# Optimization experiments

Hardware: AMD Instinct MI355X
Metric: run time of the kernel (lower is better)

The kernel has to match this reference:

```python
import jax, jax.numpy as jnp
import numpy as np

U, I, D, E = 100000, 50000, 128, 3200000


def setup_inputs() -> dict:
    key = jax.random.key(0)
    k0, k1, k2, k3, k4 = jax.random.split(key, 5)
    stdv = 1.0 / np.sqrt(D)
    return {
        "user_embedding": jax.random.uniform(k0, (U, D), jnp.float32, -stdv, stdv),
        "item_embedding": jax.random.uniform(k1, (I, D), jnp.float32, -stdv, stdv),
        "edge_vals": jax.random.uniform(k2, (E,), jnp.float32),  # normalized adj values
        "edge_u": jax.random.randint(k3, (E,), 0, U, jnp.int32),
        "edge_i": jax.random.randint(k4, (E,), 0, I, jnp.int32),
        "n_layers": 3,
    }


def reference(user_embedding, item_embedding, edge_vals, edge_u, edge_i, n_layers):
    # LightGCN forward: alternate SpMM on bipartite graph G [U,I] (COO edges),
    # then average embeddings across layers 0..n_layers.
    num_users = user_embedding.shape[0]
    num_items = item_embedding.shape[0]
    u_list = [user_embedding]
    i_list = [item_embedding]
    w = edge_vals[:, None]  # [E,1]
    for layer in range(n_layers):
        # u_{l+1} = G @ i_l : gather item rows along edges, scale, scatter-add to users
        new_u = jax.ops.segment_sum(w * i_list[layer][edge_i], edge_u,
                                    num_segments=num_users)
        # i_{l+1} = G^T @ u_l
        new_i = jax.ops.segment_sum(w * u_list[layer][edge_u], edge_i,
                                    num_segments=num_items)
        u_list.append(new_u)
        i_list.append(new_i)
    denom = jnp.float32(n_layers + 1)
    embed_user = sum(u_list) / denom
    embed_item = sum(i_list) / denom
    return (embed_user, embed_item)
```

## Files before the change

### kernel.cpp

```cpp
#include <hip/hip_runtime.h>


#define D 128
#define CHUNK 8192
#define CTILE 64
#define SRCMASK 0x3FFFF
#define TPB 256
#define RS_CAP 6144
#define NSPLIT 16

typedef unsigned int u32x2 __attribute__((ext_vector_type(2)));
typedef float f32x4 __attribute__((ext_vector_type(4)));

__device__ inline uint2 ntload_u2(const uint2* p) {
    u32x2 v = __builtin_nontemporal_load((const u32x2*)p);
    uint2 r; r.x = v.x; r.y = v.y; return r;
}
__device__ inline void ntstore_f4(float* p, float4 v) {
    f32x4 t; t.x = v.x; t.y = v.y; t.z = v.z; t.w = v.w;
    __builtin_nontemporal_store(t, (f32x4*)p);
}
__device__ inline int ntload_i(const int* p) { return __builtin_nontemporal_load(p); }
__device__ inline float ntload_f(const float* p) { return __builtin_nontemporal_load(p); }
__device__ inline float4 ntload_f4(const float* p) {
    f32x4 v = __builtin_nontemporal_load((const f32x4*)p);
    return make_float4(v.x, v.y, v.z, v.w);
}

__device__ inline unsigned pack4(float a, float b, float c, float d, float qs) {
    int q0 = __float2int_rn(a * qs), q1 = __float2int_rn(b * qs);
    int q2 = __float2int_rn(c * qs), q3 = __float2int_rn(d * qs);
    return ((unsigned)(q0 & 255)) | ((unsigned)(q1 & 255) << 8) |
           ((unsigned)(q2 & 255) << 16) | ((unsigned)(q3 & 255) << 24);
}

__device__ inline void acc_q8(float4& sa, float4& sb, uint2 raw, float m) {
    unsigned x = raw.x, y = raw.y;
    sa.x += m * (float)((int)(x << 24) >> 24);
    sa.y += m * (float)((int)(x << 16) >> 24);
    sa.z += m * (float)((int)(x <<  8) >> 24);
    sa.w += m * (float)((int)(x      ) >> 24);
    sb.x += m * (float)((int)(y << 24) >> 24);
    sb.y += m * (float)((int)(y << 16) >> 24);
    sb.z += m * (float)((int)(y <<  8) >> 24);
    sb.w += m * (float)((int)(y      ) >> 24);
}

__global__ __launch_bounds__(TPB) void k_quant8(
    const float* __restrict__ ue, const float* __restrict__ ie,
    uint2* __restrict__ h0q, float* __restrict__ sc0, int U, int UA, int NP) {
    int row = blockIdx.x * (TPB / 16) + (threadIdx.x >> 4);
    if (row >= NP) return;
    int lane = threadIdx.x & 15;
    float4 a = make_float4(0.f, 0.f, 0.f, 0.f);
    float4 b = make_float4(0.f, 0.f, 0.f, 0.f);
    const float* p = nullptr;
    if (row < U)        p = ue + (size_t)row * D + lane * 8;
    else if (row >= UA) p = ie + (size_t)(row - UA) * D + lane * 8;
    if (p) { a = ntload_f4(p); b = ntload_f4(p + 4); }
    float m = fmaxf(fmaxf(fmaxf(fabsf(a.x), fabsf(a.y)), fmaxf(fabsf(a.z), fabsf(a.w))),
                    fmaxf(fmaxf(fabsf(b.x), fabsf(b.y)), fmaxf(fabsf(b.z), fabsf(b.w))));
    for (int d_ = 1; d_ < 16; d_ <<= 1) m = fmaxf(m, __shfl_xor(m, d_));
    float qs = (m > 0.f) ? 127.f / m : 0.f;
    uint2 q;
    q.x = pack4(a.x, a.y, a.z, a.w, qs);
    q.y = pack4(b.x, b.y, b.z, b.w, qs);
    h0q[(size_t)row * 16 + lane] = q;
    if (lane == 0) sc0[row] = m * (1.f / 127.f);
}

__global__ __launch_bounds__(256) void k_count(const int* __restrict__ eu,
                                               const int* __restrict__ ei,
                                               int* __restrict__ C, int* __restrict__ C2,
                                               int E, int NB, int NS, int UA) {
    extern __shared__ int hist[];
    for (int k = threadIdx.x; k < NB; k += blockDim.x) hist[k] = 0;
    __syncthreads();
    int base = blockIdx.x * CHUNK;
    int n = min(CHUNK, E - base);
    for (int t = threadIdx.x; t < n; t += blockDim.x) {
        int u = ntload_i(eu + base + t);
        int i = ntload_i(ei + base + t);
        atomicAdd(&hist[u >> 6], 1);
        atomicAdd(&hist[(UA + i) >> 6], 1);
    }
    __syncthreads();
    int* Crow = C + (size_t)blockIdx.x * NB;
    for (int k = threadIdx.x; k < NB; k += blockDim.x) Crow[k] = hist[k];
    int* C2row = C2 + (size_t)blockIdx.x * NS;
    for (int s = threadIdx.x; s < NS; s += blockDim.x) {
        int b0 = s * 64, b1 = min(b0 + 64, NB);
        int acc = 0;
        for (int b = b0; b < b1; ++b) acc += hist[b];
        C2row[s] = acc;
    }
}

__global__ __launch_bounds__(256) void k_tile_sum(const int* __restrict__ C,
                                                  int* __restrict__ S, int NB, int NC) {
    int b = blockIdx.x * 256 + threadIdx.x;
    if (b >= NB) return;
    int tc = blockIdx.y;
    int c0 = tc * CTILE, c1 = min(c0 + CTILE, NC);
    int s = 0;
    for (int c = c0; c < c1; ++c) s += C[(size_t)c * NB + b];
    S[(size_t)tc * NB + b] = s;
}

__global__ __launch_bounds__(256) void k_super(int* __restrict__ S, int* __restrict__ T,
                                               int NB, int TC) {
    int b = blockIdx.x * 256 + threadIdx.x;
    if (b >= NB) return;
    int run = 0;
    for (int tc = 0; tc < TC; ++tc) {
        size_t k = (size_t)tc * NB + b;
        int v = S[k];
        S[k] = run;
        run += v;
    }
    T[b] = run;
}

__global__ __launch_bounds__(1024) void k_scan(const int* __restrict__ T,
                                               int* __restrict__ offb, int N) {
    __shared__ int partial[1024];
    int t = threadIdx.x;
    int CH = (N + 1023) >> 10;
    int c0 = min(t * CH, N), c1 = min(c0 + CH, N);
    int sum = 0;
    for (int k = c0; k < c1; ++k) sum += T[k];
    partial[t] = sum;
    __syncthreads();
    for (int s = 1; s < 1024; s <<= 1) {
        int add = (t >= s) ? partial[t - s] : 0;
        __syncthreads();
        partial[t] += add;
        __syncthreads();
    }
    int run = (t == 0) ? 0 : partial[t - 1];
    for (int k = c0; k < c1; ++k) { offb[k] = run; run += T[k]; }
    if (t == 0) offb[N] = partial[1023];
}

__global__ __launch_bounds__(256) void k_colscan(const int* __restrict__ C,
                                                 const int* __restrict__ S,
                                                 const int* __restrict__ offb,
                                                 int* __restrict__ colScan, int NB, int NC) {
    int b = blockIdx.x * 256 + threadIdx.x;
    if (b >= NB) return;
    int tc = blockIdx.y;
    int c0 = tc * CTILE, c1 = min(c0 + CTILE, NC);
    int run = offb[b] + S[(size_t)tc * NB + b];
    for (int c = c0; c < c1; ++c) {
        size_t k = (size_t)c * NB + b;
        colScan[k] = run;
        run += C[k];
    }
}

__global__ __launch_bounds__(256) void k_split(
    const int* __restrict__ eu, const int* __restrict__ ei, const float* __restrict__ w,
    const int* __restrict__ C2, int* __restrict__ P2, uint2* __restrict__ sbA,
    int E, int NC, int NS, int UA) {
    __shared__ int cur[64];
    __shared__ int tmp[64];
    int t = threadIdx.x;
    int c = blockIdx.x;
    if (c >= NC) return;
    if (t < NS) tmp[t] = C2[(size_t)c * NS + t];
    __syncthreads();
    if (t == 0) {
        int run = c * 2 * CHUNK;
        for (int s = 0; s < NS; ++s) {
            int v = tmp[s];
            cur[s] = run;
            P2[(size_t)c * NS + s] = run;
            run += v;
        }
    }
    __syncthreads();
    int base = c * CHUNK;
    int n = min(CHUNK, E - base);
    for (int k = t; k < n; k += 256) {
        int u  = ntload_i(eu + base + k);
        int gi = UA + ntload_i(ei + base + k);
        unsigned wb = __float_as_uint(ntload_f(w + base + k));
        int pu = atomicAdd(&cur[u >> 12], 1);
        sbA[pu] = make_uint2(((unsigned)(u & 4095) << 18) | (unsigned)gi, wb);
        int pi = atomicAdd(&cur[gi >> 12], 1);
        sbA[pi] = make_uint2(((unsigned)(gi & 4095) << 18) | (unsigned)u, wb);
    }
}

__global__ __launch_bounds__(256) void k_sbscatter(
    const uint2* __restrict__ sbA, uint2* __restrict__ bkt,
    const int* __restrict__ C2, const int* __restrict__ P2,
    const int* __restrict__ colScan, int NB, int NC, int NS) {
    __shared__ int cur[64];
    int s = blockIdx.y;
    int j = blockIdx.x;
    int CL = (NC + NSPLIT - 1) / NSPLIT;
    int c0 = j * CL, c1 = min(NC, c0 + CL);
    if (c0 >= c1) return;
    int t = threadIdx.x;
    int b0 = s * 64;
    int nb = min(64, NB - b0);
    if (t < nb) cur[t] = colScan[(size_t)c0 * NB + b0 + t];
    __syncthreads();
    for (int c = c0; c < c1; ++c) {
        int start = P2[(size_t)c * NS + s];
        int len   = C2[(size_t)c * NS + s];
        for (int k = t; k < len; k += 256) {
            uint2 e = ntload_u2(sbA + start + k);
            int bl = (int)((e.x >> 24) & 63u);
            int p = atomicAdd(&cur[bl], 1);
            bkt[p] = e;
        }
    }
}

__device__ inline unsigned pack_entry(uint2 e) {
    float wv = __uint_as_float(e.y);
    int wq = __float2int_rn(wv * 16384.f);
    wq = min(wq, 16383);
    wq = max(wq, 0);
    return (e.x & 0x3FFFFu) | ((unsigned)wq << 18);
}

__global__ __launch_bounds__(256) void k_rowsort(
    const uint2* __restrict__ entA, unsigned* __restrict__ entB,
    const int* __restrict__ offb, int* __restrict__ off, int NP) {
    __shared__ int hist[64];
    __shared__ int rowOff[64];
    __shared__ int cursor[64];
    __shared__ uint2 ebuf[RS_CAP];
    int b = blockIdx.x, t = threadIdx.x;
    int segBase = offb[b];
    int len = offb[b + 1] - segBase;
    if (t < 64) hist[t] = 0;
    __syncthreads();
    if (len <= RS_CAP) {
        for (int k = t; k < len; k += 256) {
            uint2 e = ntload_u2(entA + segBase + k);
            ebuf[k] = e;
            atomicAdd(&hist[(e.x >> 18) & 63u], 1);
        }
        __syncthreads();
        if (t == 0) {
            int run = 0;
            for (int r = 0; r < 64; ++r) { rowOff[r] = run; cursor[r] = run; run += hist[r]; }
        }
        __syncthreads();
        for (int k = t; k < len; k += 256) {
            uint2 e = ebuf[k];
            int p = atomicAdd(&cursor[(e.x >> 18) & 63u], 1);
            entB[segBase + p] = pack_entry(e);
        }
    } else {
        for (int k = t; k < len; k += 256)
            atomicAdd(&hist[(ntload_u2(entA + segBase + k).x >> 18) & 63u], 1);
        __syncthreads();
        if (t == 0) {
            int run = 0;
            for (int r = 0; r < 64; ++r) { rowOff[r] = run; cursor[r] = run; run += hist[r]; }
        }
        __syncthreads();
        for (int k = t; k < len; k += 256) {
            uint2 e = ntload_u2(entA + segBase + k);
            int p = atomicAdd(&cursor[(e.x >> 18) & 63u], 1);
            entB[segBase + p] = pack_entry(e);
        }
    }
    __syncthreads();
    if (t < 64) {
        int g = b * 64 + t;
        if (g <= NP) off[g] = segBase + rowOff[t];
    }
}

#define WDEQ (1.f / 16384.f)
template <int MODE>
__global__ __launch_bounds__(TPB) void k_spmm(
    const uint2* __restrict__ q, const float* __restrict__ sc,
    uint2* __restrict__ nxtq, float* __restrict__ scn,
    const uint2* __restrict__ e1q, const float* __restrict__ sc1,
    const uint2* __restrict__ e2q, const float* __restrict__ sc2,
    const float* __restrict__ ue, const float* __restrict__ ie,
    float* __restrict__ out,
    const int* __restrict__ off, const unsigned* __restrict__ csr,
    int U, int UA, int rowBase, int rowCnt) {
    int row = rowBase + blockIdx.x * (TPB / 16) + (threadIdx.x >> 4);
    if (row >= rowBase + rowCnt) return;
    int lane = threadIdx.x & 15;
    int beg = off[row], end = off[row + 1];
    float4 sa = make_float4(0.f, 0.f, 0.f, 0.f);
    float4 sb = make_float4(0.f, 0.f, 0.f, 0.f);

    int nIter = (end - beg) >> 2;
    int p = beg;
    if (nIter > 0) {
        unsigned m0 = csr[p], m1 = csr[p + 1], m2 = csr[p + 2], m3 = csr[p + 3];
        for (int it = 0; it < nIter; ++it) {
            int s0 = m0 & SRCMASK, s1 = m1 & SRCMASK;
            int s2 = m2 & SRCMASK, s3 = m3 & SRCMASK;
            uint2 g0 = q[(size_t)s0 * 16 + lane];
            uint2 g1 = q[(size_t)s1 * 16 + lane];
            uint2 g2 = q[(size_t)s2 * 16 + lane];
            uint2 g3 = q[(size_t)s3 * 16 + lane];
            float f0 = (float)(m0 >> 18) * WDEQ * sc[s0];
            float f1 = (float)(m1 >> 18) * WDEQ * sc[s1];
            float f2 = (float)(m2 >> 18) * WDEQ * sc[s2];
            float f3 = (float)(m3 >> 18) * WDEQ * sc[s3];
            int pn = p + 4;
            if (it + 1 < nIter) {
                m0 = csr[pn];     m1 = csr[pn + 1];
                m2 = csr[pn + 2]; m3 = csr[pn + 3];
            }
            acc_q8(sa, sb, g0, f0);
            acc_q8(sa, sb, g1, f1);
            acc_q8(sa, sb, g2, f2);
            acc_q8(sa, sb, g3, f3);
            p = pn;
        }
    }
    for (; p < end; ++p) {
        unsigned m_ = csr[p];
        int s_ = m_ & SRCMASK;
        uint2 g_ = q[(size_t)s_ * 16 + lane];
        acc_q8(sa, sb, g_, (float)(m_ >> 18) * WDEQ * sc[s_]);
    }

    if (MODE == 0) {
        float m = fmaxf(fmaxf(fmaxf(fabsf(sa.x), fabsf(sa.y)), fmaxf(fabsf(sa.z), fabsf(sa.w))),
                        fmaxf(fmaxf(fabsf(sb.x), fabsf(sb.y)), fmaxf(fabsf(sb.z), fabsf(sb.w))));
        for (int d_ = 1; d_ < 16; d_ <<= 1) m = fmaxf(m, __shfl_xor(m, d_));
        float qs = (m > 0.f) ? 127.f / m : 0.f;
        uint2 qo;
        qo.x = pack4(sa.x, sa.y, sa.z, sa.w, qs);
        qo.y = pack4(sb.x, sb.y, sb.z, sb.w, qs);
        nxtq[(size_t)row * 16 + lane] = qo;
        if (lane == 0) scn[row] = m * (1.f / 127.f);
    } else {
        int outRow;
        const float* e0p;
        if (row < U)        { outRow = row;            e0p = ue + (size_t)row * D + lane * 8; }
        else if (row >= UA) { outRow = U + (row - UA); e0p = ie + (size_t)(row - UA) * D + lane * 8; }
        else return;
        float4 e0a = ntload_f4(e0p);
        float4 e0b = ntload_f4(e0p + 4);
        uint2 q1 = e1q[(size_t)row * 16 + lane]; float s1r = sc1[row];
        uint2 q2 = e2q[(size_t)row * 16 + lane]; float s2r = sc2[row];
        unsigned x1 = q1.x, y1 = q1.y, x2 = q2.x, y2 = q2.y;
        float4 ra, rb;
        ra.x = 0.25f * (e0a.x + s1r * (float)((int)(x1 << 24) >> 24) + s2r * (float)((int)(x2 << 24) >> 24) + sa.x);
        ra.y = 0.25f * (e0a.y + s1r * (float)((int)(x1 << 16) >> 24) + s2r * (float)((int)(x2 << 16) >> 24) + sa.y);
        ra.z = 0.25f * (e0a.z + s1r * (float)((int)(x1 <<  8) >> 24) + s2r * (float)((int)(x2 <<  8) >> 24) + sa.z);
        ra.w = 0.25f * (e0a.w + s1r * (float)((int)(x1      ) >> 24) + s2r * (float)((int)(x2      ) >> 24) + sa.w);
        rb.x = 0.25f * (e0b.x + s1r * (float)((int)(y1 << 24) >> 24) + s2r * (float)((int)(y2 << 24) >> 24) + sb.x);
        rb.y = 0.25f * (e0b.y + s1r * (float)((int)(y1 << 16) >> 24) + s2r * (float)((int)(y2 << 16) >> 24) + sb.y);
        rb.z = 0.25f * (e0b.z + s1r * (float)((int)(y1 <<  8) >> 24) + s2r * (float)((int)(y2 <<  8) >> 24) + sb.z);
        rb.w = 0.25f * (e0b.w + s1r * (float)((int)(y1      ) >> 24) + s2r * (float)((int)(y2      ) >> 24) + sb.w);
        float* op = out + (size_t)outRow * D + lane * 8;
        ntstore_f4(op, ra);
        ntstore_f4(op + 4, rb);
    }
}

extern "C" void kernel_launch(void* const* d_in, const int* in_sizes, int n_in,
                              void* d_out, int out_size, void* d_ws, size_t ws_size,
                              hipStream_t stream) {
    const float* ue = (const float*)d_in[0];
    const float* ie = (const float*)d_in[1];
    const float* w  = (const float*)d_in[2];
    const int*   eu = (const int*)d_in[3];
    const int*   ei = (const int*)d_in[4];

    const int U  = in_sizes[0] / D;
    const int I  = in_sizes[1] / D;
    const int E  = in_sizes[2];
    const int UA = ((U + 63) >> 6) << 6;
    const int NP = UA + I;
    const int NB = (NP + 63) >> 6;
    const int NS = (NP + 4095) >> 12;
    const int NC = (E + CHUNK - 1) / CHUNK;
    const int TC = (NC + CTILE - 1) / CTILE;
    const size_t nE2 = (size_t)2 * E;
    const size_t nX  = (size_t)NC * 2 * CHUNK;

    uint2* h0q = (uint2*)d_ws;
    uint2* e1q = h0q + (size_t)NP * 16;
    uint2* e2q = e1q + (size_t)NP * 16;
    float* sc0 = (float*)(e2q + (size_t)NP * 16);
    float* sc1 = sc0 + NP;
    float* sc2 = sc1 + NP;
    uint2* X   = (uint2*)(sc2 + NP);
    uint2* Y   = X + nX;
    int* C       = (int*)(Y + nE2);
    int* colScan = C + (size_t)NC * NB;
    int* S       = colScan + (size_t)NC * NB;
    int* T       = S + (size_t)TC * NB;
    int* offb    = T + NB;
    int* off     = offb + NB + 1;
    int* C2      = off + NP + 1;
    int* P2      = C2 + (size_t)NC * NS;

    const size_t needed = (size_t)NP * D * 3 + (size_t)NP * 12
                        + (nX + nE2) * 8
                        + ((size_t)2 * NC * NB + (size_t)TC * NB + NB + (NB + 1)
                           + (NP + 1) + (size_t)2 * NC * NS) * 4;
    if (ws_size < needed) return;

    const int nbR = (NP + 15) / 16;
    const int nbU = (UA + 15) / 16;
    const int nbI = (I + 15) / 16;
    const int TB = (NB + 255) / 256;

    k_quant8<<<nbR, TPB, 0, stream>>>(ue, ie, h0q, sc0, U, UA, NP);
    k_count<<<NC, 256, (size_t)NB * 4, stream>>>(eu, ei, C, C2, E, NB, NS, UA);
    k_tile_sum<<<dim3(TB, TC), 256, 0, stream>>>(C, S, NB, NC);
    k_super<<<TB, 256, 0, stream>>>(S, T, NB, TC);
    k_scan<<<1, 1024, 0, stream>>>(T, offb, NB);
    k_colscan<<<dim3(TB, TC), 256, 0, stream>>>(C, S, offb, colScan, NB, NC);
    k_split<<<NC, 256, 0, stream>>>(eu, ei, w, C2, P2, X, E, NC, NS, UA);
    k_sbscatter<<<dim3(NSPLIT, NS), 256, 0, stream>>>(X, Y, C2, P2, colScan, NB, NC, NS);
    k_rowsort<<<NB, 256, 0, stream>>>(Y, (unsigned*)X, offb, off, NP);

    const unsigned* csr = (const unsigned*)X;
    k_spmm<0><<<nbU, TPB, 0, stream>>>(h0q, sc0, e1q, sc1, nullptr, nullptr, nullptr, nullptr,
                                       ue, ie, nullptr, off, csr, U, UA, 0, UA);
    k_spmm<0><<<nbI, TPB, 0, stream>>>(h0q, sc0, e1q, sc1, nullptr, nullptr, nullptr, nullptr,
                                       ue, ie, nullptr, off, csr, U, UA, UA, I);
    k_spmm<0><<<nbU, TPB, 0, stream>>>(e1q, sc1, e2q, sc2, nullptr, nullptr, nullptr, nullptr,
                                       ue, ie, nullptr, off, csr, U, UA, 0, UA);
    k_spmm<0><<<nbI, TPB, 0, stream>>>(e1q, sc1, e2q, sc2, nullptr, nullptr, nullptr, nullptr,
                                       ue, ie, nullptr, off, csr, U, UA, UA, I);
    k_spmm<1><<<nbU, TPB, 0, stream>>>(e2q, sc2, nullptr, nullptr, e1q, sc1, e2q, sc2,
                                       ue, ie, (float*)d_out, off, csr, U, UA, 0, UA);
    k_spmm<1><<<nbI, TPB, 0, stream>>>(e2q, sc2, nullptr, nullptr, e1q, sc1, e2q, sc2,
                                       ue, ie, (float*)d_out, off, csr, U, UA, UA, I);
}
```

Baseline: 567.0 us.

## Sort CSR row entries by source superblock for gather locality in SpMM

The row-sort kernel now buckets edges by a composite key (row within block, source superblock of 4096 nodes) instead of by row alone, using a parallel block-wide prefix scan over up to 2560 counters. Within each row, neighbor indices end up grouped by source region, which is meant to improve L2 and TLB locality of the embedding gathers in the six SpMM passes. In exchange the sort kernel does more LDS work (a larger histogram and a scan), and the host returns early if the number of superblocks exceeds 40.

```diff
diff --git a/kernel.cpp b/kernel.cpp
--- a/kernel.cpp
+++ b/kernel.cpp
@@ -8,6 +8,9 @@
 #define TPB 256
 #define RS_CAP 6144
 #define NSPLIT 16
+#define SBSH 12
+#define MAXNSB 40
+#define MAXKEY (64 * MAXNSB)
 
 typedef unsigned int u32x2 __attribute__((ext_vector_type(2)));
 typedef float f32x4 __attribute__((ext_vector_type(4)));
@@ -229,49 +232,57 @@
 
 __global__ __launch_bounds__(256) void k_rowsort(
     const uint2* __restrict__ entA, unsigned* __restrict__ entB,
-    const int* __restrict__ offb, int* __restrict__ off, int NP) {
-    __shared__ int hist[64];
+    const int* __restrict__ offb, int* __restrict__ off, int NP, int NSB) {
+    __shared__ int keyCnt[MAXKEY];
+    __shared__ int partial[256];
     __shared__ int rowOff[64];
-    __shared__ int cursor[64];
     __shared__ uint2 ebuf[RS_CAP];
     int b = blockIdx.x, t = threadIdx.x;
     int segBase = offb[b];
     int len = offb[b + 1] - segBase;
-    if (t < 64) hist[t] = 0;
-    __syncthreads();
-    if (len <= RS_CAP) {
-        for (int k = t; k < len; k += 256) {
-            uint2 e = ntload_u2(entA + segBase + k);
-            ebuf[k] = e;
-            atomicAdd(&hist[(e.x >> 18) & 63u], 1);
-        }
+    int NK = 64 * NSB;
+    for (int k = t; k < NK; k += 256) keyCnt[k] = 0;
+    __syncthreads();
+    bool inLds = (len <= RS_CAP);
+    for (int k = t; k < len; k += 256) {
+        uint2 e = ntload_u2(entA + segBase + k);
+        if (inLds) ebuf[k] = e;
+        int key = (int)((e.x >> 18) & 63u) * NSB + (int)((e.x & 0x3FFFFu) >> SBSH);
+        atomicAdd(&keyCnt[key], 1);
+    }
+    __syncthreads();
+    int CH = (NK + 255) >> 8;
+    int c0 = min(t * CH, NK), c1 = min(c0 + CH, NK);
+    int sum = 0;
+    for (int k = c0; k < c1; ++k) sum += keyCnt[k];
+    partial[t] = sum;
+    __syncthreads();
+    for (int s = 1; s < 256; s <<= 1) {
+        int add = (t >= s) ? partial[t - s] : 0;
         __syncthreads();
-        if (t == 0) {
-            int run = 0;
-            for (int r = 0; r < 64; ++r) { rowOff[r] = run; cursor[r] = run; run += hist[r]; }
-        }
+        partial[t] += add;
         __syncthreads();
+    }
+    int run = (t == 0) ? 0 : partial[t - 1];
+    for (int k = c0; k < c1; ++k) { int v = keyCnt[k]; keyCnt[k] = run; run += v; }
+    __syncthreads();
+    if (t < 64) rowOff[t] = keyCnt[t * NSB];
+    __syncthreads();
+    if (inLds) {
         for (int k = t; k < len; k += 256) {
             uint2 e = ebuf[k];
-            int p = atomicAdd(&cursor[(e.x >> 18) & 63u], 1);
+            int key = (int)((e.x >> 18) & 63u) * NSB + (int)((e.x & 0x3FFFFu) >> SBSH);
+            int p = atomicAdd(&keyCnt[key], 1);
             entB[segBase + p] = pack_entry(e);
         }
     } else {
-        for (int k = t; k < len; k += 256)
-            atomicAdd(&hist[(ntload_u2(entA + segBase + k).x >> 18) & 63u], 1);
-        __syncthreads();
-        if (t == 0) {
-            int run = 0;
-            for (int r = 0; r < 64; ++r) { rowOff[r] = run; cursor[r] = run; run += hist[r]; }
-        }
-        __syncthreads();
         for (int k = t; k < len; k += 256) {
             uint2 e = ntload_u2(entA + segBase + k);
-            int p = atomicAdd(&cursor[(e.x >> 18) & 63u], 1);
+            int key = (int)((e.x >> 18) & 63u) * NSB + (int)((e.x & 0x3FFFFu) >> SBSH);
+            int p = atomicAdd(&keyCnt[key], 1);
             entB[segBase + p] = pack_entry(e);
         }
     }
-    __syncthreads();
     if (t < 64) {
         int g = b * 64 + t;
         if (g <= NP) off[g] = segBase + rowOff[t];
@@ -387,6 +398,8 @@
     const size_t nE2 = (size_t)2 * E;
     const size_t nX  = (size_t)NC * 2 * CHUNK;
 
+    if (NS > MAXNSB) return;
+
     uint2* h0q = (uint2*)d_ws;
     uint2* e1q = h0q + (size_t)NP * 16;
     uint2* e2q = e1q + (size_t)NP * 16;
@@ -423,7 +436,7 @@
     k_colscan<<<dim3(TB, TC), 256, 0, stream>>>(C, S, offb, colScan, NB, NC);
     k_split<<<NC, 256, 0, stream>>>(eu, ei, w, C2, P2, X, E, NC, NS, UA);
     k_sbscatter<<<dim3(NSPLIT, NS), 256, 0, stream>>>(X, Y, C2, P2, colScan, NB, NC, NS);
-    k_rowsort<<<NB, 256, 0, stream>>>(Y, (unsigned*)X, offb, off, NP);
+    k_rowsort<<<NB, 256, 0, stream>>>(Y, (unsigned*)X, offb, off, NP, NS);
 
     const unsigned* csr = (const unsigned*)X;
     k_spmm<0><<<nbU, TPB, 0, stream>>>(h0q, sc0, e1q, sc1, nullptr, nullptr, nullptr, nullptr,
```

Result: no change. 573.1 us (+1.1%).

## Pad CSR rows to multiples of four and use offset-binary int8 with vector index loads

Applied to the files above, without the earlier changes.

The row sort now pads every row's edge list to a multiple of four with zero entries (weight zero) and adds a fixed per-block gap, so the SpMM inner loop can read edges as aligned uint4 loads with no scalar tail loop. Quantization switches from signed int8 to offset-binary uint8, so unpacking needs only masks and shifts; the constant 128 bias is removed once per row using the accumulated weight sum. This is meant to cut per-edge load and unpack instruction cost in the gather-bound SpMM kernels. The cost is extra padding writes and a new early exit when NS exceeds 64.

```diff
diff --git a/kernel.cpp b/kernel.cpp
--- a/kernel.cpp
+++ b/kernel.cpp
@@ -8,6 +8,7 @@
 #define TPB 256
 #define RS_CAP 6144
 #define NSPLIT 16
+#define PAD 192
 
 typedef unsigned int u32x2 __attribute__((ext_vector_type(2)));
 typedef float f32x4 __attribute__((ext_vector_type(4)));
@@ -28,22 +29,23 @@
 }
 
 __device__ inline unsigned pack4(float a, float b, float c, float d, float qs) {
-    int q0 = __float2int_rn(a * qs), q1 = __float2int_rn(b * qs);
-    int q2 = __float2int_rn(c * qs), q3 = __float2int_rn(d * qs);
+    int q0 = __float2int_rn(fmaf(a, qs, 128.f)), q1 = __float2int_rn(fmaf(b, qs, 128.f));
+    int q2 = __float2int_rn(fmaf(c, qs, 128.f)), q3 = __float2int_rn(fmaf(d, qs, 128.f));
     return ((unsigned)(q0 & 255)) | ((unsigned)(q1 & 255) << 8) |
            ((unsigned)(q2 & 255) << 16) | ((unsigned)(q3 & 255) << 24);
 }
 
-__device__ inline void acc_q8(float4& sa, float4& sb, uint2 raw, float m) {
+__device__ inline void acc_u8(float4& sa, float4& sb, uint2 raw, float f, float& F) {
     unsigned x = raw.x, y = raw.y;
-    sa.x += m * (float)((int)(x << 24) >> 24);
-    sa.y += m * (float)((int)(x << 16) >> 24);
-    sa.z += m * (float)((int)(x <<  8) >> 24);
-    sa.w += m * (float)((int)(x      ) >> 24);
-    sb.x += m * (float)((int)(y << 24) >> 24);
-    sb.y += m * (float)((int)(y << 16) >> 24);
-    sb.z += m * (float)((int)(y <<  8) >> 24);
-    sb.w += m * (float)((int)(y      ) >> 24);
+    sa.x = fmaf(f, (float)(x & 255u),         sa.x);
+    sa.y = fmaf(f, (float)((x >> 8) & 255u),  sa.y);
+    sa.z = fmaf(f, (float)((x >> 16) & 255u), sa.z);
+    sa.w = fmaf(f, (float)(x >> 24),          sa.w);
+    sb.x = fmaf(f, (float)(y & 255u),         sb.x);
+    sb.y = fmaf(f, (float)((y >> 8) & 255u),  sb.y);
+    sb.z = fmaf(f, (float)((y >> 16) & 255u), sb.z);
+    sb.w = fmaf(f, (float)(y >> 24),          sb.w);
+    F += f;
 }
 
 __global__ __launch_bounds__(TPB) void k_quant8(
@@ -229,53 +231,60 @@
 
 __global__ __launch_bounds__(256) void k_rowsort(
     const uint2* __restrict__ entA, unsigned* __restrict__ entB,
-    const int* __restrict__ offb, int* __restrict__ off, int NP) {
+    const int* __restrict__ offb, int* __restrict__ off, int NP, int NB) {
     __shared__ int hist[64];
     __shared__ int rowOff[64];
     __shared__ int cursor[64];
+    __shared__ int padTot;
     __shared__ uint2 ebuf[RS_CAP];
     int b = blockIdx.x, t = threadIdx.x;
     int segBase = offb[b];
     int len = offb[b + 1] - segBase;
+    int outBase = segBase + PAD * b;
     if (t < 64) hist[t] = 0;
     __syncthreads();
-    if (len <= RS_CAP) {
-        for (int k = t; k < len; k += 256) {
-            uint2 e = ntload_u2(entA + segBase + k);
-            ebuf[k] = e;
-            atomicAdd(&hist[(e.x >> 18) & 63u], 1);
-        }
-        __syncthreads();
-        if (t == 0) {
-            int run = 0;
-            for (int r = 0; r < 64; ++r) { rowOff[r] = run; cursor[r] = run; run += hist[r]; }
-        }
-        __syncthreads();
+    bool inLds = (len <= RS_CAP);
+    for (int k = t; k < len; k += 256) {
+        uint2 e = ntload_u2(entA + segBase + k);
+        if (inLds) ebuf[k] = e;
+        atomicAdd(&hist[(e.x >> 18) & 63u], 1);
+    }
+    __syncthreads();
+    if (t == 0) {
+        int run = 0;
+        for (int r = 0; r < 64; ++r) {
+            rowOff[r] = run; cursor[r] = run;
+            run += (hist[r] + 3) & ~3;
+        }
+        padTot = run;
+    }
+    __syncthreads();
+    if (inLds) {
         for (int k = t; k < len; k += 256) {
             uint2 e = ebuf[k];
             int p = atomicAdd(&cursor[(e.x >> 18) & 63u], 1);
-            entB[segBase + p] = pack_entry(e);
+            entB[outBase + p] = pack_entry(e);
         }
     } else {
-        for (int k = t; k < len; k += 256)
-            atomicAdd(&hist[(ntload_u2(entA + segBase + k).x >> 18) & 63u], 1);
-        __syncthreads();
-        if (t == 0) {
-            int run = 0;
-            for (int r = 0; r < 64; ++r) { rowOff[r] = run; cursor[r] = run; run += hist[r]; }
-        }
-        __syncthreads();
         for (int k = t; k < len; k += 256) {
             uint2 e = ntload_u2(entA + segBase + k);
             int p = atomicAdd(&cursor[(e.x >> 18) & 63u], 1);
-            entB[segBase + p] = pack_entry(e);
-        }
-    }
-    __syncthreads();
+            entB[outBase + p] = pack_entry(e);
+        }
+    }
+    __syncthreads();
+    if (t < 64) {
+        int start = rowOff[t] + hist[t];
+        int end_  = rowOff[t] + ((hist[t] + 3) & ~3);
+        for (int k = start; k < end_; ++k) entB[outBase + k] = 0u;
+    }
+    int nextBase = offb[b + 1] + PAD * (b + 1);
+    for (int k = outBase + padTot + t; k < nextBase; k += 256) entB[k] = 0u;
     if (t < 64) {
         int g = b * 64 + t;
-        if (g <= NP) off[g] = segBase + rowOff[t];
-    }
+        if (g <= NP) off[g] = outBase + rowOff[t];
+    }
+    if (b == NB - 1 && t == 0 && NP == NB * 64) off[NP] = outBase + padTot;
 }
 
 #define WDEQ (1.f / 16384.f)
@@ -295,12 +304,14 @@
     int beg = off[row], end = off[row + 1];
     float4 sa = make_float4(0.f, 0.f, 0.f, 0.f);
     float4 sb = make_float4(0.f, 0.f, 0.f, 0.f);
-
-    int nIter = (end - beg) >> 2;
-    int p = beg;
-    if (nIter > 0) {
-        unsigned m0 = csr[p], m1 = csr[p + 1], m2 = csr[p + 2], m3 = csr[p + 3];
-        for (int it = 0; it < nIter; ++it) {
+    float F = 0.f;
+
+    int n4 = (end - beg) >> 2;
+    const uint4* cp = (const uint4*)(csr + beg);
+    if (n4 > 0) {
+        uint4 e = cp[0];
+        for (int it = 0; it < n4; ++it) {
+            unsigned m0 = e.x, m1 = e.y, m2 = e.z, m3 = e.w;
             int s0 = m0 & SRCMASK, s1 = m1 & SRCMASK;
             int s2 = m2 & SRCMASK, s3 = m3 & SRCMASK;
             uint2 g0 = q[(size_t)s0 * 16 + lane];
@@ -311,24 +322,16 @@
             float f1 = (float)(m1 >> 18) * WDEQ * sc[s1];
             float f2 = (float)(m2 >> 18) * WDEQ * sc[s2];
             float f3 = (float)(m3 >> 18) * WDEQ * sc[s3];
-            int pn = p + 4;
-            if (it + 1 < nIter) {
-                m0 = csr[pn];     m1 = csr[pn + 1];
-                m2 = csr[pn + 2]; m3 = csr[pn + 3];
-            }
-            acc_q8(sa, sb, g0, f0);
-            acc_q8(sa, sb, g1, f1);
-            acc_q8(sa, sb, g2, f2);
-            acc_q8(sa, sb, g3, f3);
-            p = pn;
-        }
-    }
-    for (; p < end; ++p) {
-        unsigned m_ = csr[p];
-        int s_ = m_ & SRCMASK;
-        uint2 g_ = q[(size_t)s_ * 16 + lane];
-        acc_q8(sa, sb, g_, (float)(m_ >> 18) * WDEQ * sc[s_]);
-    }
+            e = cp[min(it + 1, n4 - 1)];
+            acc_u8(sa, sb, g0, f0, F);
+            acc_u8(sa, sb, g1, f1, F);
+            acc_u8(sa, sb, g2, f2, F);
+            acc_u8(sa, sb, g3, f3, F);
+        }
+    }
+    float c128 = 128.f * F;
+    sa.x -= c128; sa.y -= c128; sa.z -= c128; sa.w -= c128;
+    sb.x -= c128; sb.y -= c128; sb.z -= c128; sb.w -= c128;
 
     if (MODE == 0) {
         float m = fmaxf(fmaxf(fmaxf(fabsf(sa.x), fabsf(sa.y)), fmaxf(fabsf(sa.z), fabsf(sa.w))),
@@ -352,14 +355,14 @@
         uint2 q2 = e2q[(size_t)row * 16 + lane]; float s2r = sc2[row];
         unsigned x1 = q1.x, y1 = q1.y, x2 = q2.x, y2 = q2.y;
         float4 ra, rb;
-        ra.x = 0.25f * (e0a.x + s1r * (float)((int)(x1 << 24) >> 24) + s2r * (float)((int)(x2 << 24) >> 24) + sa.x);
-        ra.y = 0.25f * (e0a.y + s1r * (float)((int)(x1 << 16) >> 24) + s2r * (float)((int)(x2 << 16) >> 24) + sa.y);
-        ra.z = 0.25f * (e0a.z + s1r * (float)((int)(x1 <<  8) >> 24) + s2r * (float)((int)(x2 <<  8) >> 24) + sa.z);
-        ra.w = 0.25f * (e0a.w + s1r * (float)((int)(x1      ) >> 24) + s2r * (float)((int)(x2      ) >> 24) + sa.w);
-        rb.x = 0.25f * (e0b.x + s1r * (float)((int)(y1 << 24) >> 24) + s2r * (float)((int)(y2 << 24) >> 24) + sb.x);
-        rb.y = 0.25f * (e0b.y + s1r * (float)((int)(y1 << 16) >> 24) + s2r * (float)((int)(y2 << 16) >> 24) + sb.y);
-        rb.z = 0.25f * (e0b.z + s1r * (float)((int)(y1 <<  8) >> 24) + s2r * (float)((int)(y2 <<  8) >> 24) + sb.z);
-        rb.w = 0.25f * (e0b.w + s1r * (float)((int)(y1      ) >> 24) + s2r * (float)((int)(y2      ) >> 24) + sb.w);
+        ra.x = 0.25f * (e0a.x + s1r * ((float)(x1 & 255u) - 128.f)         + s2r * ((float)(x2 & 255u) - 128.f)         + sa.x);
+        ra.y = 0.25f * (e0a.y + s1r * ((float)((x1 >> 8) & 255u) - 128.f)  + s2r * ((float)((x2 >> 8) & 255u) - 128.f)  + sa.y);
+        ra.z = 0.25f * (e0a.z + s1r * ((float)((x1 >> 16) & 255u) - 128.f) + s2r * ((float)((x2 >> 16) & 255u) - 128.f) + sa.z);
+        ra.w = 0.25f * (e0a.w + s1r * ((float)(x1 >> 24) - 128.f)          + s2r * ((float)(x2 >> 24) - 128.f)          + sa.w);
+        rb.x = 0.25f * (e0b.x + s1r * ((float)(y1 & 255u) - 128.f)         + s2r * ((float)(y2 & 255u) - 128.f)         + sb.x);
+        rb.y = 0.25f * (e0b.y + s1r * ((float)((y1 >> 8) & 255u) - 128.f)  + s2r * ((float)((y2 >> 8) & 255u) - 128.f)  + sb.y);
+        rb.z = 0.25f * (e0b.z + s1r * ((float)((y1 >> 16) & 255u) - 128.f) + s2r * ((float)((y2 >> 16) & 255u) - 128.f) + sb.z);
+        rb.w = 0.25f * (e0b.w + s1r * ((float)(y1 >> 24) - 128.f)          + s2r * ((float)(y2 >> 24) - 128.f)          + sb.w);
         float* op = out + (size_t)outRow * D + lane * 8;
         ntstore_f4(op, ra);
         ntstore_f4(op + 4, rb);
@@ -386,6 +389,8 @@
     const int TC = (NC + CTILE - 1) / CTILE;
     const size_t nE2 = (size_t)2 * E;
     const size_t nX  = (size_t)NC * 2 * CHUNK;
+
+    if (NS > 64) return;
 
     uint2* h0q = (uint2*)d_ws;
     uint2* e1q = h0q + (size_t)NP * 16;
@@ -423,7 +428,7 @@
     k_colscan<<<dim3(TB, TC), 256, 0, stream>>>(C, S, offb, colScan, NB, NC);
     k_split<<<NC, 256, 0, stream>>>(eu, ei, w, C2, P2, X, E, NC, NS, UA);
     k_sbscatter<<<dim3(NSPLIT, NS), 256, 0, stream>>>(X, Y, C2, P2, colScan, NB, NC, NS);
-    k_rowsort<<<NB, 256, 0, stream>>>(Y, (unsigned*)X, offb, off, NP);
+    k_rowsort<<<NB, 256, 0, stream>>>(Y, (unsigned*)X, offb, off, NP, NB);
 
     const unsigned* csr = (const unsigned*)X;
     k_spmm<0><<<nbU, TPB, 0, stream>>>(h0q, sc0, e1q, sc1, nullptr, nullptr, nullptr, nullptr,
```

Result: slower. 683.3 us (+20.5%).
